# Kernel tuning notes

Measured on AMD Instinct MI355X. Metric: run time of the kernel, lower is better.

Reference implementation:

```python
import jax, jax.numpy as jnp
import numpy as np

D_MODEL = 1024
NHEAD = 16
D_K = D_MODEL // NHEAD


def setup_inputs() -> dict:
    key = jax.random.key(0)
    ks = jax.random.split(key, 8)
    B, S = 2, 2048
    scale = 1.0 / np.sqrt(D_MODEL)
    return {
        "Q": jax.random.normal(ks[0], (B, S, D_MODEL), dtype=jnp.float32),
        "K": jax.random.normal(ks[1], (B, S, D_MODEL), dtype=jnp.float32),
        "V": jax.random.normal(ks[2], (B, S, D_MODEL), dtype=jnp.float32),
        "WQ": jax.random.normal(ks[3], (D_MODEL, D_MODEL), dtype=jnp.float32) * scale,
        "WK": jax.random.normal(ks[4], (D_MODEL, D_MODEL), dtype=jnp.float32) * scale,
        "WV": jax.random.normal(ks[5], (D_MODEL, D_MODEL), dtype=jnp.float32) * scale,
        "Wfc": jax.random.normal(ks[6], (D_MODEL, D_MODEL), dtype=jnp.float32) * scale,
        "bfc": jax.random.normal(ks[7], (D_MODEL,), dtype=jnp.float32) * 0.01,
    }


def reference(Q, K, V, WQ, WK, WV, Wfc, bfc):
    B, Sq, _ = Q.shape
    Skv = K.shape[1]
    # Linear projections (torch Linear: x @ W^T), split into heads: [B, H, S, d_k]
    q = (Q @ WQ.T).reshape(B, Sq, NHEAD, D_K).transpose(0, 2, 1, 3)
    k = (K @ WK.T).reshape(B, Skv, NHEAD, D_K).transpose(0, 2, 1, 3)
    v = (V @ WV.T).reshape(B, Skv, NHEAD, D_K).transpose(0, 2, 1, 3)
    # Scaled dot-product scores: [B, H, Sq, Skv]
    scores = jnp.einsum("bhqd,bhkd->bhqk", q, k) / jnp.sqrt(jnp.float32(D_K))
    # Causal mask (strict upper triangle -> -inf)
    causal = jnp.tril(jnp.ones((Sq, Skv), dtype=bool))
    scores = jnp.where(causal, scores, -jnp.inf)
    attn = jax.nn.softmax(scores, axis=-1)
    y = jnp.einsum("bhqk,bhkd->bhqd", attn, v)
    y = y.transpose(0, 2, 1, 3).reshape(B, Sq, D_MODEL)
    return y @ Wfc.T + bfc
```

## Files before the change

### kernel.cpp

```cpp
#include <hip/hip_runtime.h>

typedef __attribute__((ext_vector_type(8))) short bf16x8;
typedef __attribute__((ext_vector_type(4))) float f32x4;
typedef __attribute__((ext_vector_type(16))) float f32x16;

__device__ __forceinline__ ushort f2bf(float f) {
    union { float f; unsigned u; } x; x.f = f;
    unsigned r = x.u + 0x7fffu + ((x.u >> 16) & 1u);
    return (ushort)(r >> 16);
}

__device__ __forceinline__ void async16(const void* g, void* l) {
    __builtin_amdgcn_global_load_lds(
        (const __attribute__((address_space(1))) void*)g,
        (__attribute__((address_space(3))) void*)l, 16, 0, 0);
}

__device__ __forceinline__ f32x4 mfma16(bf16x8 a, bf16x8 b, f32x4 c) {
    return __builtin_amdgcn_mfma_f32_16x16x32_bf16(a, b, c, 0, 0, 0);
}
__device__ __forceinline__ f32x16 mfma32(bf16x8 a, bf16x8 b, f32x16 c) {
    return __builtin_amdgcn_mfma_f32_32x32x16_bf16(a, b, c, 0, 0, 0);
}

__device__ __forceinline__ f32x4 zero4() { f32x4 z = {0.f, 0.f, 0.f, 0.f}; return z; }

__device__ __forceinline__ float xhalf_max(float v) {
    return fmaxf(v, __shfl_xor(v, 32));
}
__device__ __forceinline__ float xhalf_sum(float v) {
    return v + __shfl_xor(v, 32);
}

#define PIPE_BARRIER(cond_more)                                          \
    do {                                                                 \
        if (cond_more) asm volatile("s_waitcnt vmcnt(4)" ::: "memory");  \
        else           asm volatile("s_waitcnt vmcnt(0)" ::: "memory");  \
        asm volatile("s_waitcnt lgkmcnt(0)" ::: "memory");               \
        __builtin_amdgcn_sched_barrier(0);                               \
        __builtin_amdgcn_s_barrier();                                    \
        __builtin_amdgcn_sched_barrier(0);                               \
    } while (0)

#define END_BARRIER()                                                    \
    do {                                                                 \
        asm volatile("s_waitcnt lgkmcnt(0)" ::: "memory");               \
        __builtin_amdgcn_sched_barrier(0);                               \
        __builtin_amdgcn_s_barrier();                                    \
        __builtin_amdgcn_sched_barrier(0);                               \
    } while (0)

__global__ void cvt7_kernel(
    const float* __restrict__ s0, const float* __restrict__ s1, const float* __restrict__ s2,
    const float* __restrict__ s3, const float* __restrict__ s4, const float* __restrict__ s5,
    const float* __restrict__ s6,
    ushort* __restrict__ d0, ushort* __restrict__ d1, ushort* __restrict__ d2,
    ushort* __restrict__ d3, ushort* __restrict__ d4, ushort* __restrict__ d5,
    ushort* __restrict__ d6)
{
    int y = blockIdx.y;
    const float* s; ushort* d; int n4;
    if      (y == 0) { s = s0; d = d0; n4 = 1048576; }
    else if (y == 1) { s = s1; d = d1; n4 = 1048576; }
    else if (y == 2) { s = s2; d = d2; n4 = 1048576; }
    else if (y == 3) { s = s3; d = d3; n4 = 262144; }
    else if (y == 4) { s = s4; d = d4; n4 = 262144; }
    else if (y == 5) { s = s5; d = d5; n4 = 262144; }
    else             { s = s6; d = d6; n4 = 262144; }
    int i = blockIdx.x * 256 + threadIdx.x;
    if (i >= n4) return;
    float4 v = ((const float4*)s)[i];
    ushort4 o;
    o.x = f2bf(v.x); o.y = f2bf(v.y); o.z = f2bf(v.z); o.w = f2bf(v.w);
    ((ushort4*)d)[i] = o;
}

template<bool SWAP>
__device__ __forceinline__ void gemm_core(
    const ushort* __restrict__ A, const ushort* __restrict__ W,
    char* smem, int bm, int bn, int tid, f32x4 acc[4][4])
{
    const int lane = tid & 63;
    const int wid  = tid >> 6;
    const int wr = wid >> 1, wc = wid & 1;
    const int l15 = lane & 15, g = lane >> 4;

    auto stage = [&](int kt) {
        char* As = smem + (kt % 3) * 16384;
        char* Bs = As + 8192;
        #pragma unroll
        for (int it = 0; it < 2; ++it) {
            int c = it * 256 + tid;
            int row = c >> 2, inner = c & 3;
            int srcoff = (inner ^ (row & 3)) * 16;
            async16((const char*)A + (size_t)(bm * 128 + row) * 2048 + kt * 64 + srcoff, As + c * 16);
            async16((const char*)W + (size_t)(bn * 128 + row) * 2048 + kt * 64 + srcoff, Bs + c * 16);
        }
    };

    stage(0);
    stage(1);

    for (int kt = 0; kt < 32; ++kt) {
        PIPE_BARRIER(kt < 31);
        if (kt < 30) stage(kt + 2);

        const char* As = smem + (kt % 3) * 16384;
        const char* Bs = As + 8192;
        bf16x8 af[4], bfr[4];
        #pragma unroll
        for (int mt = 0; mt < 4; ++mt) {
            int row = wr * 64 + mt * 16 + l15;
            af[mt] = *(const bf16x8*)(As + ((row * 64 + g * 16) ^ ((row & 3) << 4)));
        }
        #pragma unroll
        for (int nt = 0; nt < 4; ++nt) {
            int row = wc * 64 + nt * 16 + l15;
            bfr[nt] = *(const bf16x8*)(Bs + ((row * 64 + g * 16) ^ ((row & 3) << 4)));
        }
        __builtin_amdgcn_s_setprio(1);
        #pragma unroll
        for (int mt = 0; mt < 4; ++mt)
            #pragma unroll
            for (int nt = 0; nt < 4; ++nt) {
                if (SWAP) acc[mt][nt] = mfma16(bfr[nt], af[mt], acc[mt][nt]);
                else      acc[mt][nt] = mfma16(af[mt], bfr[nt], acc[mt][nt]);
            }
        __builtin_amdgcn_s_setprio(0);
    }
}

__global__ __launch_bounds__(256, 2) void gemm_qkv(
    const ushort* __restrict__ Qb, const ushort* __restrict__ Kb, const ushort* __restrict__ Vb,
    const ushort* __restrict__ WQ, const ushort* __restrict__ WK, const ushort* __restrict__ WV,
    ushort* __restrict__ qhb, ushort* __restrict__ khb, ushort* __restrict__ vhT)
{
    __shared__ __align__(16) char smem[49152];
    const int tid = threadIdx.x;
    const int z  = blockIdx.x % 3;
    const int bm = blockIdx.x / 3;
    const int bn = blockIdx.y;
    const int lane = tid & 63;
    const int wid  = tid >> 6;
    const int wr = wid >> 1, wc = wid & 1;
    const int l15 = lane & 15, g = lane >> 4;

    const ushort* A  = (z == 0) ? Qb : (z == 1) ? Kb : Vb;
    const ushort* Wm = (z == 0) ? WQ : (z == 1) ? WK : WV;

    f32x4 acc[4][4];
    #pragma unroll
    for (int i = 0; i < 4; ++i)
        #pragma unroll
        for (int j = 0; j < 4; ++j) acc[i][j] = zero4();

    if (z == 2) {
        gemm_core<true>(A, Wm, smem, bm, bn, tid, acc);
        #pragma unroll
        for (int mt = 0; mt < 4; ++mt)
            #pragma unroll
            for (int nt = 0; nt < 4; ++nt)
                #pragma unroll
                for (int j = 0; j < 4; ++j) {
                    int n = bn * 128 + wc * 64 + nt * 16 + g * 4 + j;
                    int m = bm * 128 + wr * 64 + mt * 16 + l15;
                    int b = m >> 11, s = m & 2047, h = (n >> 6) & 15, d = n & 63;
                    vhT[(((size_t)(b * 16 + h)) * 64 + d) * 2048 + s] = f2bf(acc[mt][nt][j]);
                }
    } else {
        gemm_core<false>(A, Wm, smem, bm, bn, tid, acc);
        const float scale = (z == 0) ? 0.18033688011112042f : 1.0f;
        ushort* outb = (z == 0) ? qhb : khb;
        #pragma unroll
        for (int mt = 0; mt < 4; ++mt)
            #pragma unroll
            for (int nt = 0; nt < 4; ++nt)
                #pragma unroll
                for (int j = 0; j < 4; ++j) {
                    int m = bm * 128 + wr * 64 + mt * 16 + g * 4 + j;
                    int n = bn * 128 + wc * 64 + nt * 16 + l15;
                    int b = m >> 11, s = m & 2047, h = n >> 6, d = n & 63;
                    outb[(((size_t)(b * 16 + h)) * 2048 + s) * 64 + d] = f2bf(acc[mt][nt][j] * scale);
                }
    }
}

__global__ __launch_bounds__(256, 2) void gemm_fc(
    const ushort* __restrict__ A, const ushort* __restrict__ W,
    float* __restrict__ outf, const float* __restrict__ bias)
{
    __shared__ __align__(16) char smem[49152];
    const int tid = threadIdx.x;
    const int lane = tid & 63;
    const int wid  = tid >> 6;
    const int wr = wid >> 1, wc = wid & 1;
    const int l15 = lane & 15, g = lane >> 4;

    f32x4 acc[4][4];
    #pragma unroll
    for (int i = 0; i < 4; ++i)
        #pragma unroll
        for (int j = 0; j < 4; ++j) acc[i][j] = zero4();

    gemm_core<false>(A, W, smem, blockIdx.x, blockIdx.y, tid, acc);

    #pragma unroll
    for (int mt = 0; mt < 4; ++mt)
        #pragma unroll
        for (int nt = 0; nt < 4; ++nt)
            #pragma unroll
            for (int j = 0; j < 4; ++j) {
                int m = blockIdx.x * 128 + wr * 64 + mt * 16 + g * 4 + j;
                int n = blockIdx.y * 128 + wc * 64 + nt * 16 + l15;
                outf[(size_t)m * 1024 + n] = acc[mt][nt][j] + bias[n];
            }
}

__global__ __launch_bounds__(512) void attn_kernel(
    const ushort* __restrict__ qh, const ushort* __restrict__ kh,
    const ushort* __restrict__ vhT, ushort* __restrict__ yb)
{
    __shared__ __align__(16) char smem[65536];
    const int tid = threadIdx.x;
    const int lane = tid & 63, wid = tid >> 6;
    const int l31 = lane & 31;
    const int hi  = lane >> 5;
    const int group = wid >> 2;
    const int wq    = wid & 3;
    const int subkv = group * 64;
    const int id = blockIdx.x;
    const int bh = (id & 7) * 4 + ((id >> 3) & 3);
    const int qx = id >> 5;
    const size_t base = (size_t)bh * 2048 * 64;
    const int b_ = bh >> 4, h_ = bh & 15;
    float* oml = (float*)smem;

    auto stageK = [&](int t, int b) {
        char* Ks = smem + b * 32768;
        #pragma unroll
        for (int it = 0; it < 2; ++it) {
            int c = it * 512 + tid;
            int row = c >> 3, inner = c & 7;
            async16((const char*)kh + (base + (size_t)(t * 128 + row) * 64) * 2 + ((inner ^ (row & 7)) * 16),
                    Ks + c * 16);
        }
    };
    auto stageV = [&](int t, int b) {
        char* Vs = smem + b * 32768 + 16384;
        #pragma unroll
        for (int it = 0; it < 2; ++it) {
            int c = it * 512 + tid;
            int row = c >> 4, inner = c & 15;
            async16((const char*)vhT + (base + (size_t)row * 2048 + (size_t)t * 128) * 2 + ((inner ^ (row & 15)) * 16),
                    Vs + c * 16);
        }
    };

    for (int p = 0; p < 2; ++p) {
        const int qt  = (p == 0) ? qx : 15 - qx;
        const int qrw = qt * 128 + wq * 32;

        bf16x8 qf[4];
        #pragma unroll
        for (int ks = 0; ks < 4; ++ks)
            qf[ks] = *(const bf16x8*)((const char*)qh + (base + (size_t)(qrw + l31) * 64) * 2 + ks * 32 + hi * 16);

        f32x16 o[2];
        #pragma unroll
        for (int r = 0; r < 16; ++r) { o[0][r] = 0.f; o[1][r] = 0.f; }
        float m_run = -1e30f, l_run = 0.f;

        stageK(0, 0); stageV(0, 0);

        for (int t = 0; t <= qt; ++t) {
            const bool more = (t + 1 <= qt);
            if (more) { stageK(t + 1, (t + 1) & 1); stageV(t + 1, (t + 1) & 1); }
            PIPE_BARRIER(more);

            const int kv0 = t * 128 + subkv;
            if (kv0 <= qrw + 31) {
                const char* Ks = smem + (t & 1) * 32768;
                const char* Vs = Ks + 16384;

                bf16x8 kf[2][4];
                #pragma unroll
                for (int tt = 0; tt < 2; ++tt)
                    #pragma unroll
                    for (int ks = 0; ks < 4; ++ks) {
                        int krow = subkv + tt * 32 + l31;
                        int byte = (krow * 128 + ks * 32 + hi * 16) ^ ((krow & 7) << 4);
                        kf[tt][ks] = *(const bf16x8*)(Ks + byte);
                    }

                f32x16 st[2];
                #pragma unroll
                for (int r = 0; r < 16; ++r) { st[0][r] = 0.f; st[1][r] = 0.f; }
                __builtin_amdgcn_s_setprio(1);
                #pragma unroll
                for (int tt = 0; tt < 2; ++tt)
                    #pragma unroll
                    for (int ks = 0; ks < 4; ++ks)
                        st[tt] = mfma32(kf[tt][ks], qf[ks], st[tt]);
                __builtin_amdgcn_s_setprio(0);

                bf16x8 vf[4][2];
                #pragma unroll
                for (int ks = 0; ks < 4; ++ks)
                    #pragma unroll
                    for (int dt = 0; dt < 2; ++dt) {
                        int vrow = dt * 32 + l31;
                        int colB = subkv * 2 + ks * 32 + hi * 16;
                        int byte = vrow * 256 + (colB ^ ((vrow & 15) << 4));
                        vf[ks][dt] = *(const bf16x8*)(Vs + byte);
                    }

                if (kv0 + 63 > qrw) {
                    #pragma unroll
                    for (int tt = 0; tt < 2; ++tt)
                        #pragma unroll
                        for (int r = 0; r < 16; ++r) {
                            int kv = kv0 + tt * 32 + (r & 3) + 8 * (r >> 2) + 4 * hi;
                            if (kv > qrw + l31) st[tt][r] = -1e30f;
                        }
                }

                float mx;
                {
                    float t0[8];
                    #pragma unroll
                    for (int r = 0; r < 8; ++r)
                        t0[r] = fmaxf(fmaxf(st[0][r], st[0][r + 8]),
                                      fmaxf(st[1][r], st[1][r + 8]));
                    float t1[4];
                    #pragma unroll
                    for (int r = 0; r < 4; ++r) t1[r] = fmaxf(t0[r], t0[r + 4]);
                    float t2a = fmaxf(t1[0], t1[2]), t2b = fmaxf(t1[1], t1[3]);
                    mx = fmaxf(t2a, t2b);
                }
                mx = xhalf_max(mx);

                if (!__all(mx - m_run <= 8.0f)) {
                    float mn = fmaxf(m_run, mx);
                    float corr = __builtin_amdgcn_exp2f(m_run - mn);
                    l_run *= corr;
                    m_run = mn;
                    #pragma unroll
                    for (int r = 0; r < 16; ++r) {
                        int qsrc = (r & 3) + 8 * (r >> 2) + 4 * hi;
                        float c2 = __shfl(corr, qsrc);
                        o[0][r] *= c2; o[1][r] *= c2;
                    }
                }

                #pragma unroll
                for (int tt = 0; tt < 2; ++tt)
                    #pragma unroll
                    for (int r = 0; r < 16; ++r)
                        st[tt][r] = __builtin_amdgcn_exp2f(st[tt][r] - m_run);
                float sum;
                {
                    float s0[8];
                    #pragma unroll
                    for (int r = 0; r < 8; ++r)
                        s0[r] = (st[0][r] + st[0][r + 8]) + (st[1][r] + st[1][r + 8]);
                    float s1[4];
                    #pragma unroll
                    for (int r = 0; r < 4; ++r) s1[r] = s0[r] + s0[r + 4];
                    sum = (s1[0] + s1[2]) + (s1[1] + s1[3]);
                }
                sum = xhalf_sum(sum);
                l_run += sum;

                unsigned Wd[2][8], Xw[2][8];
                #pragma unroll
                for (int tt = 0; tt < 2; ++tt)
                    #pragma unroll
                    for (int k = 0; k < 8; ++k) {
                        unsigned w;
                        asm("v_cvt_pk_bf16_f32 %0, %1, %2" : "=v"(w) : "v"(st[tt][2 * k]), "v"(st[tt][2 * k + 1]));
                        Wd[tt][k] = w;
                    }
                #pragma unroll
                for (int tt = 0; tt < 2; ++tt)
                    #pragma unroll
                    for (int k = 0; k < 8; ++k)
                        Xw[tt][k] = __shfl_xor((int)Wd[tt][k], 32);

                #pragma unroll
                for (int ks = 0; ks < 4; ++ks) {
                    const int t2 = ks >> 1, bse = (ks & 1) * 4;
                    unsigned w0 = hi ? Xw[t2][bse + 2] : Wd[t2][bse + 0];
                    unsigned w1 = hi ? Xw[t2][bse + 3] : Wd[t2][bse + 1];
                    unsigned w2 = hi ? Wd[t2][bse + 2] : Xw[t2][bse + 0];
                    unsigned w3 = hi ? Wd[t2][bse + 3] : Xw[t2][bse + 1];
                    unsigned pw4[4] = {w0, w1, w2, w3};
                    bf16x8 pf = *(const bf16x8*)pw4;
                    __builtin_amdgcn_s_setprio(1);
                    #pragma unroll
                    for (int dt = 0; dt < 2; ++dt)
                        o[dt] = mfma32(pf, vf[ks][dt], o[dt]);
                    __builtin_amdgcn_s_setprio(0);
                }
            }
            END_BARRIER();
        }

        if (group == 1) {
            float* pp = oml + (size_t)(wq * 64 + lane) * 36;
            #pragma unroll
            for (int r = 0; r < 16; ++r) { pp[r] = o[0][r]; pp[16 + r] = o[1][r]; }
            pp[32] = m_run; pp[33] = l_run;
        }
        __syncthreads();
        if (group == 0) {
            const float* pp = oml + (size_t)(wq * 64 + lane) * 36;
            float m1 = pp[32], l1 = pp[33];
            float mn = fmaxf(m_run, m1);
            float a0 = __builtin_amdgcn_exp2f(m_run - mn);
            float a1 = __builtin_amdgcn_exp2f(m1 - mn);
            float lt = l_run * a0 + l1 * a1;
            float invl = 1.0f / lt;
            #pragma unroll
            for (int r = 0; r < 16; ++r) {
                int qsrc = (r & 3) + 8 * (r >> 2) + 4 * hi;
                float f0 = __shfl(a0, qsrc);
                float f1 = __shfl(a1, qsrc);
                float iv = __shfl(invl, qsrc);
                float v0 = (o[0][r] * f0 + pp[r] * f1) * iv;
                float v1 = (o[1][r] * f0 + pp[16 + r] * f1) * iv;
                int q = qrw + qsrc;
                size_t rowoff = ((size_t)(b_ * 2048 + q)) * 1024 + h_ * 64;
                yb[rowoff + l31]      = f2bf(v0);
                yb[rowoff + 32 + l31] = f2bf(v1);
            }
        }
        __syncthreads();
    }
}

extern "C" void kernel_launch(void* const* d_in, const int* in_sizes, int n_in,
                              void* d_out, int out_size, void* d_ws, size_t ws_size,
                              hipStream_t stream)
{
    const size_t MD = 4096ull * 1024;
    const size_t WD = 1024ull * 1024;
    ushort* ws  = (ushort*)d_ws;
    ushort* Qb  = ws;
    ushort* Kb  = Qb + MD;
    ushort* Vb  = Kb + MD;
    ushort* qhb = Vb + MD;
    ushort* khb = qhb + MD;
    ushort* vhT = khb + MD;
    ushort* WQb = vhT + MD;
    ushort* WKb = WQb + WD;
    ushort* WVb = WKb + WD;
    ushort* Wfb = WVb + WD;
    ushort* yb  = Qb;

    cvt7_kernel<<<dim3(4096, 7), 256, 0, stream>>>(
        (const float*)d_in[0], (const float*)d_in[1], (const float*)d_in[2],
        (const float*)d_in[3], (const float*)d_in[4], (const float*)d_in[5],
        (const float*)d_in[6],
        Qb, Kb, Vb, WQb, WKb, WVb, Wfb);

    gemm_qkv<<<dim3(96, 8), 256, 0, stream>>>(Qb, Kb, Vb, WQb, WKb, WVb, qhb, khb, vhT);
    attn_kernel<<<256, 512, 0, stream>>>(qhb, khb, vhT, yb);
    gemm_fc<<<dim3(32, 8), 256, 0, stream>>>(yb, Wfb, (float*)d_out, (const float*)d_in[7]);
}
```

Measured before the change: 108.6 us.

## Double attention block to 1024 threads with four KV groups and 256-wide tiles

The attention kernel now runs 16 waves per block instead of 8. Four KV sub-groups each handle a 64-column slice of a 256-wide KV tile, so each block makes half as many pipeline iterations per query tile. LDS staging doubles to 128KB and the final merge combines four partial softmax states instead of two. In exchange, the per-thread register budget is halved (risk of spills), only one block fits per CU, and the coarser KV tile does more masked work along the causal diagonal.

```diff
diff --git a/kernel.cpp b/kernel.cpp
--- a/kernel.cpp
+++ b/kernel.cpp
@@ -216,11 +216,11 @@
             }
 }
 
-__global__ __launch_bounds__(512) void attn_kernel(
+__global__ __launch_bounds__(1024, 4) void attn_kernel(
     const ushort* __restrict__ qh, const ushort* __restrict__ kh,
     const ushort* __restrict__ vhT, ushort* __restrict__ yb)
 {
-    __shared__ __align__(16) char smem[65536];
+    __shared__ __align__(16) char smem[131072];
     const int tid = threadIdx.x;
     const int lane = tid & 63, wid = tid >> 6;
     const int l31 = lane & 31;
@@ -236,22 +236,22 @@
     float* oml = (float*)smem;
 
     auto stageK = [&](int t, int b) {
-        char* Ks = smem + b * 32768;
+        char* Ks = smem + b * 65536;
         #pragma unroll
         for (int it = 0; it < 2; ++it) {
-            int c = it * 512 + tid;
+            int c = it * 1024 + tid;
             int row = c >> 3, inner = c & 7;
-            async16((const char*)kh + (base + (size_t)(t * 128 + row) * 64) * 2 + ((inner ^ (row & 7)) * 16),
+            async16((const char*)kh + (base + (size_t)(t * 256 + row) * 64) * 2 + ((inner ^ (row & 7)) * 16),
                     Ks + c * 16);
         }
     };
     auto stageV = [&](int t, int b) {
-        char* Vs = smem + b * 32768 + 16384;
+        char* Vs = smem + b * 65536 + 32768;
         #pragma unroll
         for (int it = 0; it < 2; ++it) {
-            int c = it * 512 + tid;
-            int row = c >> 4, inner = c & 15;
-            async16((const char*)vhT + (base + (size_t)row * 2048 + (size_t)t * 128) * 2 + ((inner ^ (row & 15)) * 16),
+            int c = it * 1024 + tid;
+            int row = c >> 5, inner = c & 31;
+            async16((const char*)vhT + (base + (size_t)row * 2048 + (size_t)t * 256) * 2 + ((inner ^ (row & 15)) * 16),
                     Vs + c * 16);
         }
     };
@@ -259,6 +259,7 @@
     for (int p = 0; p < 2; ++p) {
         const int qt  = (p == 0) ? qx : 15 - qx;
         const int qrw = qt * 128 + wq * 32;
+        const int nkv = (qt >> 1) + 1;
 
         bf16x8 qf[4];
         #pragma unroll
@@ -272,15 +273,15 @@
 
         stageK(0, 0); stageV(0, 0);
 
-        for (int t = 0; t <= qt; ++t) {
-            const bool more = (t + 1 <= qt);
+        for (int t = 0; t < nkv; ++t) {
+            const bool more = (t + 1 < nkv);
             if (more) { stageK(t + 1, (t + 1) & 1); stageV(t + 1, (t + 1) & 1); }
             PIPE_BARRIER(more);
 
-            const int kv0 = t * 128 + subkv;
+            const int kv0 = t * 256 + subkv;
             if (kv0 <= qrw + 31) {
-                const char* Ks = smem + (t & 1) * 32768;
-                const char* Vs = Ks + 16384;
+                const char* Ks = smem + (t & 1) * 65536;
+                const char* Vs = Ks + 32768;
 
                 bf16x8 kf[2][4];
                 #pragma unroll
@@ -309,8 +310,7 @@
                     #pragma unroll
                     for (int dt = 0; dt < 2; ++dt) {
                         int vrow = dt * 32 + l31;
-                        int colB = subkv * 2 + ks * 32 + hi * 16;
-                        int byte = vrow * 256 + (colB ^ ((vrow & 15) << 4));
+                        int byte = (vrow * 512 + subkv * 2 + ks * 32 + hi * 16) ^ ((vrow & 15) << 4);
                         vf[ks][dt] = *(const bf16x8*)(Vs + byte);
                     }
 
@@ -405,29 +405,37 @@
             END_BARRIER();
         }
 
-        if (group == 1) {
-            float* pp = oml + (size_t)(wq * 64 + lane) * 36;
+        if (group != 0) {
+            float* pp = oml + (size_t)((group - 1) * 256 + wq * 64 + lane) * 36;
             #pragma unroll
             for (int r = 0; r < 16; ++r) { pp[r] = o[0][r]; pp[16 + r] = o[1][r]; }
             pp[32] = m_run; pp[33] = l_run;
         }
         __syncthreads();
         if (group == 0) {
-            const float* pp = oml + (size_t)(wq * 64 + lane) * 36;
-            float m1 = pp[32], l1 = pp[33];
-            float mn = fmaxf(m_run, m1);
+            const float* p1 = oml + (size_t)(0 * 256 + wq * 64 + lane) * 36;
+            const float* p2 = oml + (size_t)(1 * 256 + wq * 64 + lane) * 36;
+            const float* p3 = oml + (size_t)(2 * 256 + wq * 64 + lane) * 36;
+            float m1 = p1[32], l1 = p1[33];
+            float m2 = p2[32], l2 = p2[33];
+            float m3 = p3[32], l3 = p3[33];
+            float mn = fmaxf(fmaxf(m_run, m1), fmaxf(m2, m3));
             float a0 = __builtin_amdgcn_exp2f(m_run - mn);
             float a1 = __builtin_amdgcn_exp2f(m1 - mn);
-            float lt = l_run * a0 + l1 * a1;
+            float a2 = __builtin_amdgcn_exp2f(m2 - mn);
+            float a3 = __builtin_amdgcn_exp2f(m3 - mn);
+            float lt = l_run * a0 + l1 * a1 + l2 * a2 + l3 * a3;
             float invl = 1.0f / lt;
             #pragma unroll
             for (int r = 0; r < 16; ++r) {
                 int qsrc = (r & 3) + 8 * (r >> 2) + 4 * hi;
                 float f0 = __shfl(a0, qsrc);
                 float f1 = __shfl(a1, qsrc);
+                float f2 = __shfl(a2, qsrc);
+                float f3 = __shfl(a3, qsrc);
                 float iv = __shfl(invl, qsrc);
-                float v0 = (o[0][r] * f0 + pp[r] * f1) * iv;
-                float v1 = (o[1][r] * f0 + pp[16 + r] * f1) * iv;
+                float v0 = (o[0][r] * f0 + p1[r] * f1 + p2[r] * f2 + p3[r] * f3) * iv;
+                float v1 = (o[1][r] * f0 + p1[16 + r] * f1 + p2[16 + r] * f2 + p3[16 + r] * f3) * iv;
                 int q = qrw + qsrc;
                 size_t rowoff = ((size_t)(b_ * 2048 + q)) * 1024 + h_ * 64;
                 yb[rowoff + l31]      = f2bf(v0);
@@ -464,6 +472,6 @@
         Qb, Kb, Vb, WQb, WKb, WVb, Wfb);
 
     gemm_qkv<<<dim3(96, 8), 256, 0, stream>>>(Qb, Kb, Vb, WQb, WKb, WVb, qhb, khb, vhT);
-    attn_kernel<<<256, 512, 0, stream>>>(qhb, khb, vhT, yb);
+    attn_kernel<<<256, 1024, 0, stream>>>(qhb, khb, vhT, yb);
     gemm_fc<<<dim3(32, 8), 256, 0, stream>>>(yb, Wfb, (float*)d_out, (const float*)d_in[7]);
 }
```

Result: slower. 182.6 us (+68.1%).
